# Kernel optimization log

Measured on AMD Instinct MI355X. Metric: run time of the kernel, lower is better.

The kernel has to match this reference:

```python
import jax, jax.numpy as jnp
import numpy as np

B, C, H, W, K = 4, 64, 512, 512, 8


def _unfold_rearrange(t, k):
    # nn.Unfold(k, stride=k) then rearrange 'b (c w h) n -> b (w h) (c n)'
    Bb, Cc, Hh, Ww = t.shape
    nh, nw = Hh // k, Ww // k
    t = t.reshape(Bb, Cc, nh, k, nw, k)
    # -> (B, kh, kw, C, ph, pw)
    t = t.transpose(0, 3, 5, 1, 2, 4)
    return t.reshape(Bb, k * k, Cc * nh * nw)


def setup_inputs() -> dict:
    key = jax.random.key(0)
    x = jax.random.normal(key, (B, C, H, W), dtype=jnp.float32)
    nh, nw = H // K, W // K
    # checkerboard over window grid -> exactly half the windows are ones per batch
    win = ((jnp.arange(nh)[:, None] + jnp.arange(nw)[None, :]) % 2 == 0)
    mask = jnp.repeat(jnp.repeat(win.astype(jnp.float32), K, axis=0), K, axis=1)
    mask = jnp.broadcast_to(mask[None, None], (B, 1, H, W)).astype(jnp.float32)
    return {"mask": mask, "x": x, "window_size": K}


def reference(mask, x, window_size):
    k = window_size
    Bb, Cc, Hh, Ww = x.shape
    N = (Hh // k) * (Ww // k)
    m = _unfold_rearrange(mask, k)          # (B, k*k, N)  (mask has C=1; expand is redundant across C)
    xr = _unfold_rearrange(x, k)            # (B, k*k, C*N)
    colmask = jnp.any(m > 0, axis=1)        # (B, N) : window has any mask
    colmask = jnp.broadcast_to(colmask[:, None, :], (Bb, Cc, N)).reshape(Bb, Cc * N)
    # stable compaction: ones-columns first (original column order preserved, matching
    # torch boolean indexing), zeros-columns after
    order = jnp.argsort(jnp.where(colmask, 0, 1).astype(jnp.int32), axis=-1, stable=True)
    M = (Cc * N) // 2                       # exactly half by mask construction
    components_ones = jnp.take_along_axis(xr, order[:, :M][:, None, :], axis=2)
    components_zeros = jnp.take_along_axis(xr, order[:, M:][:, None, :], axis=2)
    return components_ones, components_zeros
```

## Files before the change

kernel.cpp:

```cpp
#include <hip/hip_runtime.h>
#include <hip/hip_bf16.h>

#define KWIN 8
constexpr int BB = 4, CC = 64, HH = 512, WW = 512;
constexpr int NH = HH / KWIN;
constexpr int NW = WW / KWIN;
constexpr int NWIN = NH * NW;
constexpr int MCOL = (CC * NWIN) / 2;
constexpr size_t ZOFF = (size_t)BB * KWIN * KWIN * MCOL;

__global__ __launch_bounds__(1024) void compute_ranks(
    const float* __restrict__ mask, int* __restrict__ rankPacked,
    int* __restrict__ OnOut) {
  const int b = blockIdx.x;
  const int t = threadIdx.x;
  const int lane = t & 63;
  const int wid = t >> 6;
  __shared__ int waveSums[16];

  int flags[4];
  int cnt = 0;
#pragma unroll
  for (int i = 0; i < 4; ++i) {
    int n = t * 4 + i;
    int ph = n >> 6, pw = n & 63;
    const float* base = mask + ((size_t)b * HH + ph * KWIN) * WW + pw * KWIN;
    bool any = false;
#pragma unroll
    for (int kh = 0; kh < KWIN; ++kh) {
      const float4* rp = (const float4*)(base + (size_t)kh * WW);
      float4 a = rp[0], q = rp[1];
      any = any || a.x > 0.f || a.y > 0.f || a.z > 0.f || a.w > 0.f ||
            q.x > 0.f || q.y > 0.f || q.z > 0.f || q.w > 0.f;
    }
    flags[i] = any ? 1 : 0;
    cnt += flags[i];
  }

  int inc = cnt;
#pragma unroll
  for (int off = 1; off < 64; off <<= 1) {
    int up = __shfl_up(inc, off);
    if (lane >= off) inc += up;
  }
  if (lane == 63) waveSums[wid] = inc;
  __syncthreads();
  if (wid == 0 && lane < 16) {
    int v = waveSums[lane];
#pragma unroll
    for (int off = 1; off < 16; off <<= 1) {
      int up = __shfl_up(v, off);
      if (lane >= off) v += up;
    }
    waveSums[lane] = v;
  }
  __syncthreads();
  int waveOff = (wid == 0) ? 0 : waveSums[wid - 1];
  int run = waveOff + inc - cnt;
#pragma unroll
  for (int i = 0; i < 4; ++i) {
    int n = t * 4 + i;
    rankPacked[b * NWIN + n] =
        (int)((unsigned)run | (flags[i] ? 0x80000000u : 0u));
    run += flags[i];
  }
  if (t == 1023) OnOut[b] = run;
}

__device__ __forceinline__ int swz(int w) {
  return w ^ (((w >> 6) & 7) << 2);
}

__global__ __launch_bounds__(256) void scatter_perm(
    const float* __restrict__ x, const int* __restrict__ rankPacked,
    const int* __restrict__ OnArr, float* __restrict__ out) {
  const int bid = blockIdx.x;
  const int ph = bid & (NH - 1);
  const int c = (bid >> 6) & (CC - 1);
  const int b = bid >> 12;
  const int t = threadIdx.x;

  __shared__ float lds[KWIN * WW];
  __shared__ int s_pw[NW];
  __shared__ int s_meta[4];

  const float4* src =
      (const float4*)(x + ((size_t)(b * CC + c) * HH + ph * KWIN) * WW);
#pragma unroll
  for (int v = 0; v < 4; ++v) {
    int i = v * 256 + t;
    float4 val = src[i];
    int kh = i >> 7;
    int w = (i & 127) << 2;
    *(float4*)&lds[kh * WW + swz(w)] = val;
  }

  if (t < NW) {
    unsigned rp = (unsigned)rankPacked[b * NWIN + ph * NW + t];
    int flag = (int)(rp >> 31);
    int rank = (int)(rp & 0x7fffffffu);
    unsigned long long bal = __ballot(flag);
    int cntOnes = __popcll(bal);
    int below = __popcll(bal & ((1ull << t) - 1ull));
    if (flag) s_pw[below] = t;
    else s_pw[cntOnes + (t - below)] = t;
    if (t == 0) {
      s_meta[0] = cntOnes;
      s_meta[1] = rank;
      s_meta[2] = ph * NW - rank;
      s_meta[3] = OnArr[b];
    }
  }
  __syncthreads();

  const int cntOnes = s_meta[0];
  const int baseOnes = s_meta[1];
  const int baseZeros = s_meta[2];
  const int On = s_meta[3];
  const int Oz = NWIN - On;
  const bool al1 = ((c * On + baseOnes) & 3) == 0;
  const bool al2 = ((c * Oz + baseZeros) & 3) == 0;

#pragma unroll
  for (int v = 0; v < 4; ++v) {
    int idx = v * 256 + t;
    int r = idx >> 4;
    int j0 = (idx & 15) << 2;
    int kh = r >> 3, kw = r & 7;

    float vals[4];
#pragma unroll
    for (int u = 0; u < 4; ++u) {
      int pw = s_pw[j0 + u];
      vals[u] = lds[kh * WW + swz(pw * KWIN + kw)];
    }

    size_t rowOff = (size_t)(b * (KWIN * KWIN) + r) * MCOL;
    if (j0 + 3 < cntOnes) {
      float* p = out + rowOff + (size_t)c * On + (baseOnes + j0);
      if (al1)
        *(float4*)p = make_float4(vals[0], vals[1], vals[2], vals[3]);
      else {
        p[0] = vals[0]; p[1] = vals[1]; p[2] = vals[2]; p[3] = vals[3];
      }
    } else if (j0 >= cntOnes) {
      float* p = out + ZOFF + rowOff + (size_t)c * Oz +
                 (baseZeros + (j0 - cntOnes));
      if (al2)
        *(float4*)p = make_float4(vals[0], vals[1], vals[2], vals[3]);
      else {
        p[0] = vals[0]; p[1] = vals[1]; p[2] = vals[2]; p[3] = vals[3];
      }
    } else {
#pragma unroll
      for (int u = 0; u < 4; ++u) {
        int j = j0 + u;
        if (j < cntOnes)
          out[rowOff + (size_t)c * On + (baseOnes + j)] = vals[u];
        else
          out[ZOFF + rowOff + (size_t)c * Oz +
              (baseZeros + (j - cntOnes))] = vals[u];
      }
    }
  }
}

extern "C" void kernel_launch(void* const* d_in, const int* in_sizes, int n_in,
                              void* d_out, int out_size, void* d_ws,
                              size_t ws_size, hipStream_t stream) {
  const float* mask = (const float*)d_in[0];
  const float* x = (const float*)d_in[1];
  float* out = (float*)d_out;

  int* rankPacked = (int*)d_ws;
  int* OnArr = rankPacked + BB * NWIN;

  compute_ranks<<<BB, 1024, 0, stream>>>(mask, rankPacked, OnArr);
  scatter_perm<<<BB * CC * NH, 256, 0, stream>>>(x, rankPacked, OnArr, out);
}
```

Measured before the change: 508.0 us.

## Parallelize mask flags per row and process four window-rows per scatter block

The single-block-per-batch rank kernel becomes a row_flags kernel with one 64-thread block per window row, each storing a 64-bit ballot mask. The scatter kernel computes the prefix ranks itself from those masks. Each scatter block now covers four window rows with 512 threads, and global loads are staged in registers before the LDS writes. This removes the serial rank kernel's latency and raises bytes in flight per block, at the cost of redundant prefix scans per block, more LDS per block and per-store alignment checks.

```diff
diff --git a/kernel.cpp b/kernel.cpp
--- a/kernel.cpp
+++ b/kernel.cpp
@@ -8,145 +8,124 @@
 constexpr int NWIN = NH * NW;
 constexpr int MCOL = (CC * NWIN) / 2;
 constexpr size_t ZOFF = (size_t)BB * KWIN * KWIN * MCOL;
-
-__global__ __launch_bounds__(1024) void compute_ranks(
-    const float* __restrict__ mask, int* __restrict__ rankPacked,
-    int* __restrict__ OnOut) {
-  const int b = blockIdx.x;
-  const int t = threadIdx.x;
-  const int lane = t & 63;
-  const int wid = t >> 6;
-  __shared__ int waveSums[16];
-
-  int flags[4];
-  int cnt = 0;
-#pragma unroll
-  for (int i = 0; i < 4; ++i) {
-    int n = t * 4 + i;
-    int ph = n >> 6, pw = n & 63;
-    const float* base = mask + ((size_t)b * HH + ph * KWIN) * WW + pw * KWIN;
-    bool any = false;
-#pragma unroll
-    for (int kh = 0; kh < KWIN; ++kh) {
-      const float4* rp = (const float4*)(base + (size_t)kh * WW);
-      float4 a = rp[0], q = rp[1];
-      any = any || a.x > 0.f || a.y > 0.f || a.z > 0.f || a.w > 0.f ||
-            q.x > 0.f || q.y > 0.f || q.z > 0.f || q.w > 0.f;
-    }
-    flags[i] = any ? 1 : 0;
-    cnt += flags[i];
-  }
-
-  int inc = cnt;
-#pragma unroll
-  for (int off = 1; off < 64; off <<= 1) {
-    int up = __shfl_up(inc, off);
-    if (lane >= off) inc += up;
-  }
-  if (lane == 63) waveSums[wid] = inc;
-  __syncthreads();
-  if (wid == 0 && lane < 16) {
-    int v = waveSums[lane];
-#pragma unroll
-    for (int off = 1; off < 16; off <<= 1) {
-      int up = __shfl_up(v, off);
-      if (lane >= off) v += up;
-    }
-    waveSums[lane] = v;
-  }
-  __syncthreads();
-  int waveOff = (wid == 0) ? 0 : waveSums[wid - 1];
-  int run = waveOff + inc - cnt;
-#pragma unroll
-  for (int i = 0; i < 4; ++i) {
-    int n = t * 4 + i;
-    rankPacked[b * NWIN + n] =
-        (int)((unsigned)run | (flags[i] ? 0x80000000u : 0u));
-    run += flags[i];
-  }
-  if (t == 1023) OnOut[b] = run;
-}
+constexpr int PHG = 4;
 
 __device__ __forceinline__ int swz(int w) {
   return w ^ (((w >> 6) & 7) << 2);
 }
 
-__global__ __launch_bounds__(256) void scatter_perm(
-    const float* __restrict__ x, const int* __restrict__ rankPacked,
-    const int* __restrict__ OnArr, float* __restrict__ out) {
+__global__ __launch_bounds__(64) void row_flags(
+    const float* __restrict__ mask, unsigned long long* __restrict__ rowMask) {
+  const int ph = blockIdx.x & (NH - 1);
+  const int b = blockIdx.x >> 6;
+  const int pw = threadIdx.x;
+  const float* base = mask + ((size_t)b * HH + ph * KWIN) * WW + pw * KWIN;
+  bool any = false;
+#pragma unroll
+  for (int kh = 0; kh < KWIN; ++kh) {
+    const float4* rp = (const float4*)(base + (size_t)kh * WW);
+    float4 a = rp[0], q = rp[1];
+    any = any || a.x > 0.f || a.y > 0.f || a.z > 0.f || a.w > 0.f ||
+          q.x > 0.f || q.y > 0.f || q.z > 0.f || q.w > 0.f;
+  }
+  unsigned long long bal = __ballot(any);
+  if (pw == 0) rowMask[blockIdx.x] = bal;
+}
+
+__global__ __launch_bounds__(512) void scatter_perm(
+    const float* __restrict__ x, const unsigned long long* __restrict__ rowMask,
+    float* __restrict__ out) {
   const int bid = blockIdx.x;
-  const int ph = bid & (NH - 1);
-  const int c = (bid >> 6) & (CC - 1);
-  const int b = bid >> 12;
+  const int pg = bid & (NH / PHG - 1);
+  const int c = (bid >> 4) & (CC - 1);
+  const int b = bid >> 10;
   const int t = threadIdx.x;
 
-  __shared__ float lds[KWIN * WW];
-  __shared__ int s_pw[NW];
-  __shared__ int s_meta[4];
+  __shared__ float lds[PHG * KWIN * WW];
+  __shared__ unsigned char s_pw[PHG][NW];
+  __shared__ int s_cnt[PHG], s_base1[PHG];
+  __shared__ int s_On;
 
-  const float4* src =
-      (const float4*)(x + ((size_t)(b * CC + c) * HH + ph * KWIN) * WW);
+  const float* src = x + ((size_t)(b * CC + c) * HH + pg * (PHG * KWIN)) * WW;
+  float4 stage[8];
 #pragma unroll
-  for (int v = 0; v < 4; ++v) {
-    int i = v * 256 + t;
-    float4 val = src[i];
-    int kh = i >> 7;
-    int w = (i & 127) << 2;
-    *(float4*)&lds[kh * WW + swz(w)] = val;
+  for (int vv = 0; vv < 8; ++vv) {
+    stage[vv] = ((const float4*)src)[vv * 512 + t];
   }
 
-  if (t < NW) {
-    unsigned rp = (unsigned)rankPacked[b * NWIN + ph * NW + t];
-    int flag = (int)(rp >> 31);
-    int rank = (int)(rp & 0x7fffffffu);
-    unsigned long long bal = __ballot(flag);
-    int cntOnes = __popcll(bal);
-    int below = __popcll(bal & ((1ull << t) - 1ull));
-    if (flag) s_pw[below] = t;
-    else s_pw[cntOnes + (t - below)] = t;
-    if (t == 0) {
-      s_meta[0] = cntOnes;
-      s_meta[1] = rank;
-      s_meta[2] = ph * NW - rank;
-      s_meta[3] = OnArr[b];
+  if (t < 64) {
+    unsigned long long m = rowMask[b * NH + t];
+    int cnt = __popcll(m);
+    int inc = cnt;
+#pragma unroll
+    for (int off = 1; off < 64; off <<= 1) {
+      int up = __shfl_up(inc, off);
+      if (t >= off) inc += up;
     }
+    int excl = inc - cnt;
+    int loc = t - pg * PHG;
+    if (loc >= 0 && loc < PHG) s_base1[loc] = excl;
+    if (t == 63) s_On = excl + cnt;
+  } else if (t < 320) {
+    int tt = t - 64;
+    int phl = tt >> 6, j = tt & 63;
+    unsigned long long m = rowMask[b * NH + pg * PHG + phl];
+    int flag = (int)((m >> j) & 1ull);
+    int below = __popcll(m & ((1ull << j) - 1ull));
+    int cntO = __popcll(m);
+    int pos = flag ? below : cntO + j - below;
+    s_pw[phl][pos] = (unsigned char)j;
+    if (j == 0) s_cnt[phl] = cntO;
+  }
+
+#pragma unroll
+  for (int vv = 0; vv < 8; ++vv) {
+    int i = vv * 512 + t;
+    int row = i >> 7;
+    int w = (i & 127) << 2;
+    *(float4*)&lds[row * WW + swz(w)] = stage[vv];
   }
   __syncthreads();
 
-  const int cntOnes = s_meta[0];
-  const int baseOnes = s_meta[1];
-  const int baseZeros = s_meta[2];
-  const int On = s_meta[3];
+  const int On = s_On;
   const int Oz = NWIN - On;
-  const bool al1 = ((c * On + baseOnes) & 3) == 0;
-  const bool al2 = ((c * Oz + baseZeros) & 3) == 0;
 
 #pragma unroll
-  for (int v = 0; v < 4; ++v) {
-    int idx = v * 256 + t;
-    int r = idx >> 4;
-    int j0 = (idx & 15) << 2;
+  for (int v = 0; v < 8; ++v) {
+    int idx = v * 512 + t;
+    int g = idx & 15;
+    int rlo = (idx >> 4) & 3;
+    int phl = (idx >> 6) & 3;
+    int rhi = idx >> 8;
+    int r = rhi * 4 + rlo;
     int kh = r >> 3, kw = r & 7;
+    int row = phl * KWIN + kh;
+    int j0 = g * 4;
 
     float vals[4];
 #pragma unroll
     for (int u = 0; u < 4; ++u) {
-      int pw = s_pw[j0 + u];
-      vals[u] = lds[kh * WW + swz(pw * KWIN + kw)];
+      int pw = s_pw[phl][j0 + u];
+      vals[u] = lds[row * WW + swz(pw * KWIN + kw)];
     }
 
+    int cntO = s_cnt[phl];
+    int baseO = s_base1[phl];
+    int baseZ = (pg * PHG + phl) * NW - baseO;
     size_t rowOff = (size_t)(b * (KWIN * KWIN) + r) * MCOL;
-    if (j0 + 3 < cntOnes) {
-      float* p = out + rowOff + (size_t)c * On + (baseOnes + j0);
-      if (al1)
+
+    if (j0 + 3 < cntO) {
+      long col = (long)c * On + baseO + j0;
+      float* p = out + rowOff + col;
+      if ((col & 3) == 0)
         *(float4*)p = make_float4(vals[0], vals[1], vals[2], vals[3]);
       else {
         p[0] = vals[0]; p[1] = vals[1]; p[2] = vals[2]; p[3] = vals[3];
       }
-    } else if (j0 >= cntOnes) {
-      float* p = out + ZOFF + rowOff + (size_t)c * Oz +
-                 (baseZeros + (j0 - cntOnes));
-      if (al2)
+    } else if (j0 >= cntO) {
+      long col = (long)c * Oz + baseZ + (j0 - cntO);
+      float* p = out + ZOFF + rowOff + col;
+      if ((col & 3) == 0)
         *(float4*)p = make_float4(vals[0], vals[1], vals[2], vals[3]);
       else {
         p[0] = vals[0]; p[1] = vals[1]; p[2] = vals[2]; p[3] = vals[3];
@@ -155,11 +134,11 @@
 #pragma unroll
       for (int u = 0; u < 4; ++u) {
         int j = j0 + u;
-        if (j < cntOnes)
-          out[rowOff + (size_t)c * On + (baseOnes + j)] = vals[u];
+        if (j < cntO)
+          out[rowOff + (size_t)((long)c * On + baseO + j)] = vals[u];
         else
-          out[ZOFF + rowOff + (size_t)c * Oz +
-              (baseZeros + (j - cntOnes))] = vals[u];
+          out[ZOFF + rowOff + (size_t)((long)c * Oz + baseZ + (j - cntO))] =
+              vals[u];
       }
     }
   }
@@ -171,10 +150,8 @@
   const float* mask = (const float*)d_in[0];
   const float* x = (const float*)d_in[1];
   float* out = (float*)d_out;
+  unsigned long long* rowMask = (unsigned long long*)d_ws;
 
-  int* rankPacked = (int*)d_ws;
-  int* OnArr = rankPacked + BB * NWIN;
-
-  compute_ranks<<<BB, 1024, 0, stream>>>(mask, rankPacked, OnArr);
-  scatter_perm<<<BB * CC * NH, 256, 0, stream>>>(x, rankPacked, OnArr, out);
+  row_flags<<<BB * NH, 64, 0, stream>>>(mask, rowMask);
+  scatter_perm<<<BB * CC * (NH / PHG), 512, 0, stream>>>(x, rowMask, out);
 }
```

New measurement: 458.8 us. 9.7% less time.
